# Kernel optimization log

Measured on AMD Instinct MI355X. Metric: run time of the kernel, lower is better.

Reference implementation:

```python
import jax, jax.numpy as jnp
import numpy as np

# N nodes, E edges; lmax=6 -> L=(lmax+1)^2=49; lmax_reduce=(lmax+1)//2=3 -> LR=16
# (matches hardcoded c[:, :16, :] in the torch source); M=25 is the basis size of the
# lmax=4 'middle' irreps in cg_interaction2; NY = num_y_rotations.
# node_interaction's reshape(b, basis_num, c) forces sphere_channels_reduce == hidden_channels.
N, E, L, LR, M, NY, C, H, NB = 2048, 4096, 49, 16, 25, 3, 128, 128, 128
INV_SQRT_3 = float(1.0 / np.sqrt(3.0))


def _silu(v):
    return v * jax.nn.sigmoid(v)


def setup_inputs():
    key = jax.random.key(0)
    ks = jax.random.split(key, 24)
    rn = lambda k, s, sc=1.0: (sc * jax.random.normal(k, s)).astype(jnp.float32)
    return {
        "x": rn(ks[0], (N, L, C)),
        "x_time": rn(ks[1], (1, 1)),        # forward sets x_time = None; unused
        "x_glovec": rn(ks[2], (N, LR)),
        "x_edge": rn(ks[3], (E, NB)),
        "edge_index": jax.random.randint(ks[4], (2, E), 0, N),
        "edge_vec": rn(ks[5], (E, 3)),      # unused by forward body
        "node_sh_inv": rn(ks[6], (1,)),     # unused by forward body
        "node_self": rn(ks[7], (1,)),       # unused by forward body
        # dense bilinear stand-ins for the e3nn FullyConnectedTensorProducts
        "W_cg1": rn(ks[8], (L, L, M), 0.05),
        "W_cg21": rn(ks[9], (L, M, L), 0.05),
        "W_cg22": rn(ks[10], (L, M, L), 0.05),
        # node_interaction1 MLP
        "Wn1a": rn(ks[11], (LR * (C + 1), H), (LR * (C + 1)) ** -0.5),
        "bn1a": jnp.zeros((H,), jnp.float32),
        "Wn1b": rn(ks[12], (H, LR * C), H ** -0.5),
        "bn1b": jnp.zeros((LR * C,), jnp.float32),
        # node_interaction2 MLP
        "Wn2a": rn(ks[13], (LR * (C + 1), H), (LR * (C + 1)) ** -0.5),
        "bn2a": jnp.zeros((H,), jnp.float32),
        "Wn2b": rn(ks[14], (H, LR * C), H ** -0.5),
        "bn2b": jnp.zeros((LR * C,), jnp.float32),
        # fc1_dist / fc1_edge_proj / fc2_edge
        "Wd": rn(ks[15], (NB, H), NB ** -0.5),
        "bd": jnp.zeros((H,), jnp.float32),
        "Wp1": rn(ks[16], (LR * C, H), (LR * C) ** -0.5),
        "bp1": jnp.zeros((H,), jnp.float32),
        "Wp2": rn(ks[17], (H, LR * C), H ** -0.5),
        "bp2": jnp.zeros((LR * C,), jnp.float32),
        # per-edge Wigner-style rotation buffers (geometry-derived in the original)
        "wigner": rn(ks[18], (E, NY, LR, L), L ** -0.5),      # Rotate: full -> reduced, NY taps
        "wigner_inv": rn(ks[19], (E, L, LR), LR ** -0.5),     # RotateInv: reduced -> full
        "wig_node": rn(ks[20], (E, LR, LR), LR ** -0.5),      # Rotate_edge / Rotate_edgeInv
    }


def _forward(x, x_glovec, x_edge, W_cg1, W_cg21, W_cg22, Wn1a, bn1a, Wn1b, bn1b,
             Wn2a, bn2a, Wn2b, bn2b, Wd, bd, Wp1, bp1, Wp2, bp2,
             wigner, wigner_inv, wig_node, edge_index):
    src, dst = edge_index[0], edge_index[1]
    xe = _silu(x_edge @ Wd + bd)                              # [E,H]  fc1_dist
    xs, xt = x[src], x[dst]                                   # [E,L,C] edge gathers
    gs, gt = x_glovec[src], x_glovec[dst]                     # [E,LR]

    # cg_interaction2: mean over channels, CG bilinears, broadcast residual
    xm, ym = xs.mean(2), xt.mean(2)                           # [E,L]
    mid = jnp.einsum('ei,ej,ijo->eo', xm, ym, W_cg1)          # [E,M]  cg1
    sh_cg = xs + xt \
        + jnp.einsum('ei,ej,ijo->eo', xm, mid, W_cg21)[..., None] \
        + jnp.einsum('ei,ej,ijo->eo', ym, mid, W_cg22)[..., None]  # [E,L,C]

    def node_int(ne, ndf, Wa, ba, Wb, bb):
        # Rotate_edgeInv (transpose of per-edge rotation) on reduced basis
        ne = jnp.einsum('eji,ejc->eic', wig_node, ne[:, :LR, :])       # [E,LR,C]
        feat = jnp.concatenate([ne, (ne.mean(2) * ndf)[..., None]], axis=2)
        h = _silu(feat.reshape(E, LR * (C + 1)) @ Wa + ba)             # node_fc1
        h = _silu(h @ Wb + bb).reshape(E, LR, C)                       # node_fc3
        return jnp.einsum('eij,ejc->eic', wig_node, h)                 # Rotate_edge

    sh = node_int(xs, gt, Wn1a, bn1a, Wn1b, bn1b) \
       + node_int(xt, gs, Wn2a, bn2a, Wn2b, bn2b)                      # [E,LR,C]
    c = sh_cg.at[:, :LR, :].add(sh)

    def rotate(z):  # sphharm.Rotate: [E,L,C] -> [E*NY, LR*C]
        return jnp.einsum('enrb,ebc->enrc', wigner, z).reshape(E * NY, LR * C)

    msg = rotate(xs) + rotate(xt) + rotate(c)
    m = _silu(msg @ Wp1 + bp1)                                # [E*NY,H] fc1_edge_proj
    m = (m.reshape(E, NY, H) * xe[:, None, :]).reshape(E * NY, H)
    m = _silu(m @ Wp2 + bp2)                                  # fc2_edge
    m = m.reshape(E, NY, LR, C).mean(1)                       # CombineYRotations
    out = jnp.einsum('ebr,erc->ebc', wigner_inv, m) * INV_SQRT_3  # RotateInv
    return out                                                # [E,L,C]


def reference(x, x_time, x_glovec, x_edge, edge_index, edge_vec, node_sh_inv,
              node_self, W_cg1, W_cg21, W_cg22, Wn1a, bn1a, Wn1b, bn1b,
              Wn2a, bn2a, Wn2b, bn2b, Wd, bd, Wp1, bp1, Wp2, bp2,
              wigner, wigner_inv, wig_node):
    # x_time / edge_vec / node_sh_inv / node_self are unused (x_time = None in source)
    return _forward(x, x_glovec, x_edge, W_cg1, W_cg21, W_cg22, Wn1a, bn1a, Wn1b,
                    bn1b, Wn2a, bn2a, Wn2b, bn2b, Wd, bd, Wp1, bp1, Wp2, bp2,
                    wigner, wigner_inv, wig_node, edge_index)
```

## Files before the change

### kernel.cpp

```cpp
#include <hip/hip_runtime.h>
#include <hip/hip_bf16.h>

typedef __hip_bfloat16 bf16;
typedef __attribute__((ext_vector_type(8))) short short8;
typedef __attribute__((ext_vector_type(4))) float f32x4;

#define NN 2048
#define EE 4096
#define LL 49
#define LRR 16
#define NYY 3
#define CC 128
#define HH 128

#define K1P 2432
#define K2P 2496

__device__ __forceinline__ float siluf(float v) { return v * (1.0f / (1.0f + __expf(-v))); }
__device__ __forceinline__ bf16 f2b(float v) { return __float2bfloat16(v); }
__device__ __forceinline__ float getc(float4 v, int i) {
  return i == 0 ? v.x : i == 1 ? v.y : i == 2 ? v.z : v.w;
}

struct TJob { const float* in; bf16* out; int K, N, Kp; };
struct TJobs { TJob j[6]; };

__global__ __launch_bounds__(256) void transpose_cvt_kernel(TJobs jobs) {
  TJob jb = jobs.j[blockIdx.y];
  int i = blockIdx.x * 256 + threadIdx.x;
  if (i < jb.N * jb.Kp) {
    int n = i / jb.Kp, k = i - n * jb.Kp;
    jb.out[i] = (k < jb.K) ? f2b(jb.in[(long)k * jb.N + n]) : f2b(0.f);
  }
}

__global__ __launch_bounds__(256) void cg_prep_kernel(
    const float* __restrict__ Wcg1, const float* __restrict__ Wcg21,
    const float* __restrict__ Wcg22, bf16* __restrict__ BT1, bf16* __restrict__ BT2) {
  int i = blockIdx.x * 256 + threadIdx.x;
  if (blockIdx.y == 0) {
    if (i < 32 * K1P) {
      int o = i / K1P, k = i - o * K1P;
      float v = (o < 25 && k < 2401) ? Wcg1[k * 25 + o] : 0.f;
      BT1[i] = f2b(v);
    }
  } else {
    if (i < 64 * K2P) {
      int o = i / K2P, k = i - o * K2P;
      float v = 0.f;
      if (o < 49) {
        if (k < 1225) v = Wcg21[k * 49 + o];
        else if (k < 2450) v = Wcg22[(k - 1225) * 49 + o];
      }
      BT2[i] = f2b(v);
    }
  }
}

__global__ __launch_bounds__(256) void node_mean_kernel(const float* __restrict__ x,
                                                        float* __restrict__ xmean) {
  int row = blockIdx.x * 4 + (threadIdx.x >> 6);
  int lane = threadIdx.x & 63;
  const float* p = x + (long)row * CC;
  float s = p[lane] + p[lane + 64];
  for (int off = 32; off > 0; off >>= 1) s += __shfl_down(s, off);
  if (lane == 0) xmean[row] = s * (1.0f / 128.0f);
}

__global__ __launch_bounds__(256) void build_p1_kernel(
    const float* __restrict__ xmean, const int* __restrict__ eidx, bf16* __restrict__ P1) {
  __shared__ float sxm[49], sym[49];
  int e = blockIdx.x, tid = threadIdx.x;
  int s = eidx[e], d = eidx[EE + e];
  if (tid < 49) { sxm[tid] = xmean[s * 49 + tid]; sym[tid] = xmean[d * 49 + tid]; }
  __syncthreads();
  for (int idx = tid; idx < K1P; idx += 256) {
    float v = 0.f;
    if (idx < 2401) { int i = idx / 49, j = idx - i * 49; v = sxm[i] * sym[j]; }
    P1[(long)e * K1P + idx] = f2b(v);
  }
}

__global__ __launch_bounds__(256) void build_p2_kernel(
    const float* __restrict__ xmean, const float* __restrict__ mid,
    const int* __restrict__ eidx, bf16* __restrict__ P2) {
  __shared__ float sxm[49], sym[49], smid[25];
  int e = blockIdx.x, tid = threadIdx.x;
  int s = eidx[e], d = eidx[EE + e];
  if (tid < 49) { sxm[tid] = xmean[s * 49 + tid]; sym[tid] = xmean[d * 49 + tid]; }
  if (tid >= 64 && tid < 89) smid[tid - 64] = mid[e * 32 + tid - 64];
  __syncthreads();
  for (int idx = tid; idx < K2P; idx += 256) {
    float v = 0.f;
    if (idx < 1225) { int i = idx / 25, m = idx - i * 25; v = sxm[i] * smid[m]; }
    else if (idx < 2450) { int kk = idx - 1225; int i = kk / 25, m = kk - i * 25; v = sym[i] * smid[m]; }
    P2[(long)e * K2P + idx] = f2b(v);
  }
}

template <int NI>
__global__ __launch_bounds__(256) void gemm_smalln(
    const bf16* __restrict__ A, const bf16* __restrict__ BT,
    float* __restrict__ C, int K) {
  __shared__ short As[64 * 64];
  __shared__ short Bs[NI * 16 * 64];
  const int tid = threadIdx.x, w = tid >> 6, lane = tid & 63;
  const int lm = lane & 15, q = lane >> 4;
  const int bm = blockIdx.x * 64;
  f32x4 acc[NI];
#pragma unroll
  for (int ni = 0; ni < NI; ++ni) acc[ni] = (f32x4){0.f, 0.f, 0.f, 0.f};
  for (int k0 = 0; k0 < K; k0 += 64) {
    __syncthreads();
#pragma unroll
    for (int it = 0; it < 2; ++it) {
      int lc = it * 256 + tid;
      int m = lc >> 3, k8 = lc & 7;
      uint4 v = *(const uint4*)((const char*)A + ((long)(bm + m) * K + k0 + k8 * 8) * 2);
      *(uint4*)&As[(m * 8 + (k8 ^ (m & 7))) * 8] = v;
    }
#pragma unroll
    for (int it = 0; it < NI / 2; ++it) {
      int lc = it * 256 + tid;
      int n = lc >> 3, k8 = lc & 7;
      uint4 v = *(const uint4*)((const char*)BT + ((long)n * K + k0 + k8 * 8) * 2);
      *(uint4*)&Bs[(n * 8 + (k8 ^ (n & 7))) * 8] = v;
    }
    __syncthreads();
#pragma unroll
    for (int ks = 0; ks < 2; ++ks) {
      short8 af = *(const short8*)&As[(w * 16 + lm) * 64 + ((ks * 4 + q) ^ (lm & 7)) * 8];
#pragma unroll
      for (int ni = 0; ni < NI; ++ni) {
        short8 bfr = *(const short8*)&Bs[(ni * 16 + lm) * 64 + ((ks * 4 + q) ^ (lm & 7)) * 8];
        acc[ni] = __builtin_amdgcn_mfma_f32_16x16x32_bf16(af, bfr, acc[ni], 0, 0, 0);
      }
    }
  }
#pragma unroll
  for (int ni = 0; ni < NI; ++ni) {
    int col = ni * 16 + lm;
#pragma unroll
    for (int r = 0; r < 4; ++r) {
      int row = bm + w * 16 + q * 4 + r;
      C[(long)row * (NI * 16) + col] = acc[ni][r];
    }
  }
}

__global__ __launch_bounds__(256) void build_feat_kernel(
    const float* __restrict__ x, const float* __restrict__ x_glovec,
    const float* __restrict__ wig_node, const int* __restrict__ eidx,
    bf16* __restrict__ featst) {
  __shared__ float wig[256];
  __shared__ float xa[2048], xb[2048], tmp[2048];
  int e = blockIdx.x, tid = threadIdx.x;
  int s = eidx[e], d = eidx[EE + e];
  wig[tid] = wig_node[e * 256 + tid];
  if (tid < 48) {
    featst[(long)e * 2112 + 2064 + tid] = f2b(0.f);
    featst[(long)(EE + e) * 2112 + 2064 + tid] = f2b(0.f);
  }
  for (int idx = tid; idx < 2048; idx += 256) {
    int l = idx >> 7, c = idx & 127;
    xa[idx] = x[((long)s * LL + l) * CC + c];
    xb[idx] = x[((long)d * LL + l) * CC + c];
  }
  __syncthreads();
  for (int idx = tid; idx < 2048; idx += 256) {
    int i = idx >> 7, c = idx & 127;
    float a = 0.f;
#pragma unroll
    for (int j = 0; j < 16; ++j) a += wig[j * 16 + i] * xa[j * 128 + c];
    tmp[idx] = a;
    featst[(long)e * 2112 + i * 129 + c] = f2b(a);
  }
  __syncthreads();
  if (tid < 16) {
    float m = 0.f;
    for (int c = 0; c < 128; ++c) m += tmp[tid * 128 + c];
    featst[(long)e * 2112 + tid * 129 + 128] = f2b(m * (1.0f / 128.0f) * x_glovec[(long)d * 16 + tid]);
  }
  __syncthreads();
  for (int idx = tid; idx < 2048; idx += 256) {
    int i = idx >> 7, c = idx & 127;
    float a = 0.f;
#pragma unroll
    for (int j = 0; j < 16; ++j) a += wig[j * 16 + i] * xb[j * 128 + c];
    tmp[idx] = a;
    featst[(long)(EE + e) * 2112 + i * 129 + c] = f2b(a);
  }
  __syncthreads();
  if (tid < 16) {
    float m = 0.f;
    for (int c = 0; c < 128; ++c) m += tmp[tid * 128 + c];
    featst[(long)(EE + e) * 2112 + tid * 129 + 128] = f2b(m * (1.0f / 128.0f) * x_glovec[(long)s * 16 + tid]);
  }
}

__global__ __launch_bounds__(256) void gemm_f32_silu(
    const float* __restrict__ A, const float* __restrict__ B,
    const float* __restrict__ bias, float* __restrict__ C, int M, int N, int K) {
  __shared__ float As[16][68];
  __shared__ float Bs[16][64];
  const int tid = threadIdx.x;
  const int bm = blockIdx.x * 64, bn = blockIdx.y * 64;
  const int tx = tid & 15, ty = tid >> 4;
  const int ar = tid >> 2, ak = (tid & 3) * 4;
  const int br = tid >> 4, bc = (tid & 15) * 4;
  float acc[4][4] = {};
  const float* Ap = A + (long)(bm + ar) * K + ak;
  const float* Bp = B + (long)br * N + bn + bc;
  for (int k0 = 0; k0 < K; k0 += 16) {
    const float4 av = *(const float4*)(Ap + k0);
    const float4 bv = *(const float4*)(Bp + (long)k0 * N);
    __syncthreads();
    As[ak + 0][ar] = av.x; As[ak + 1][ar] = av.y;
    As[ak + 2][ar] = av.z; As[ak + 3][ar] = av.w;
    *(float4*)&Bs[br][bc] = bv;
    __syncthreads();
#pragma unroll
    for (int k = 0; k < 16; ++k) {
      const float4 a = *(const float4*)&As[k][ty * 4];
      const float4 b = *(const float4*)&Bs[k][tx * 4];
      acc[0][0] += a.x * b.x; acc[0][1] += a.x * b.y; acc[0][2] += a.x * b.z; acc[0][3] += a.x * b.w;
      acc[1][0] += a.y * b.x; acc[1][1] += a.y * b.y; acc[1][2] += a.y * b.z; acc[1][3] += a.y * b.w;
      acc[2][0] += a.z * b.x; acc[2][1] += a.z * b.y; acc[2][2] += a.z * b.z; acc[2][3] += a.z * b.w;
      acc[3][0] += a.w * b.x; acc[3][1] += a.w * b.y; acc[3][2] += a.w * b.z; acc[3][3] += a.w * b.w;
    }
  }
#pragma unroll
  for (int i = 0; i < 4; ++i) {
    int row = bm + ty * 4 + i;
#pragma unroll
    for (int j = 0; j < 4; ++j) {
      int col = bn + tx * 4 + j;
      C[(long)row * N + col] = siluf(acc[i][j] + bias[col]);
    }
  }
}

template <int BM, bool SILU, bool XE, bool OUT_BF16>
__global__ __launch_bounds__(256) void gemm_mfma(
    const bf16* __restrict__ A, const bf16* __restrict__ B0, const bf16* __restrict__ B1,
    const float* __restrict__ bias0, const float* __restrict__ bias1,
    const float* __restrict__ xe, void* __restrict__ Cout,
    int M, int N, int K, int half) {
  constexpr int MI = BM / 32;
  __shared__ short As[BM * 64];
  __shared__ short Bs[128 * 64];
  const int tid = threadIdx.x;
  const int w = tid >> 6, lane = tid & 63;
  const int lm = lane & 15, q = lane >> 4;
  const int bm = blockIdx.x * BM, bn = blockIdx.y * 128;
  const int wm = (w & 1) * (BM / 2), wn = (w >> 1) * 64;
  const bf16* Bp = (bm < half) ? B0 : B1;
  const float* bias = (bm < half) ? bias0 : bias1;

  f32x4 acc[MI][4];
#pragma unroll
  for (int mi = 0; mi < MI; ++mi)
#pragma unroll
    for (int ni = 0; ni < 4; ++ni) acc[mi][ni] = (f32x4){0.f, 0.f, 0.f, 0.f};

  for (int k0 = 0; k0 < K; k0 += 64) {
    __syncthreads();
#pragma unroll
    for (int it = 0; it < BM / 32; ++it) {
      int lc = it * 256 + tid;
      int m = lc >> 3, k8 = lc & 7;
      uint4 v = *(const uint4*)((const char*)A + ((long)(bm + m) * K + k0 + k8 * 8) * 2);
      *(uint4*)&As[(m * 8 + (k8 ^ (m & 7))) * 8] = v;
    }
#pragma unroll
    for (int it = 0; it < 4; ++it) {
      int lc = it * 256 + tid;
      int n = lc >> 3, k8 = lc & 7;
      uint4 v = *(const uint4*)((const char*)Bp + ((long)(bn + n) * K + k0 + k8 * 8) * 2);
      *(uint4*)&Bs[(n * 8 + (k8 ^ (n & 7))) * 8] = v;
    }
    __syncthreads();
#pragma unroll
    for (int ks = 0; ks < 2; ++ks) {
      short8 af[MI], bfr[4];
#pragma unroll
      for (int mi = 0; mi < MI; ++mi) {
        int row = wm + mi * 16 + lm;
        af[mi] = *(const short8*)&As[row * 64 + ((ks * 4 + q) ^ (lm & 7)) * 8];
      }
#pragma unroll
      for (int ni = 0; ni < 4; ++ni) {
        int row = wn + ni * 16 + lm;
        bfr[ni] = *(const short8*)&Bs[row * 64 + ((ks * 4 + q) ^ (lm & 7)) * 8];
      }
#pragma unroll
      for (int mi = 0; mi < MI; ++mi)
#pragma unroll
        for (int ni = 0; ni < 4; ++ni)
          acc[mi][ni] = __builtin_amdgcn_mfma_f32_16x16x32_bf16(af[mi], bfr[ni], acc[mi][ni], 0, 0, 0);
    }
  }
#pragma unroll
  for (int mi = 0; mi < MI; ++mi) {
#pragma unroll
    for (int ni = 0; ni < 4; ++ni) {
      int col = bn + wn + ni * 16 + lm;
      float bcol = bias[col];
#pragma unroll
      for (int r = 0; r < 4; ++r) {
        int row = bm + wm + mi * 16 + q * 4 + r;
        float v = acc[mi][ni][r] + bcol;
        if (SILU) v = siluf(v);
        if (XE) v *= xe[(row / 3) * HH + col];
        if (OUT_BF16) ((bf16*)Cout)[(long)row * N + col] = f2b(v);
        else ((float*)Cout)[(long)row * N + col] = v;
      }
    }
  }
}

__global__ __launch_bounds__(256) void gemm_osum(
    const bf16* __restrict__ A, const bf16* __restrict__ B0w, const bf16* __restrict__ B1w,
    const float* __restrict__ bias0, const float* __restrict__ bias1,
    float* __restrict__ osum) {
  __shared__ short As[128 * 64];
  __shared__ short Bs[128 * 64];
  const int tid = threadIdx.x;
  const int w = tid >> 6, lane = tid & 63;
  const int lm = lane & 15, q = lane >> 4;
  const int bm = blockIdx.x * 128, bn = blockIdx.y * 128;
  const int wm = (w & 1) * 64, wn = (w >> 1) * 64;
  f32x4 ov[4][4];
  f32x4 acc[4][4];
#pragma unroll
  for (int mi = 0; mi < 4; ++mi)
#pragma unroll
    for (int ni = 0; ni < 4; ++ni) acc[mi][ni] = (f32x4){0.f, 0.f, 0.f, 0.f};

#pragma unroll 1
  for (int src = 0; src < 2; ++src) {
    const bf16* Ap = A + (long)src * 4096 * 128;
    const bf16* Bp = src ? B1w : B0w;
#pragma unroll 1
    for (int k0 = 0; k0 < 128; k0 += 64) {
      __syncthreads();
#pragma unroll
      for (int it = 0; it < 4; ++it) {
        int lc = it * 256 + tid;
        int m = lc >> 3, k8 = lc & 7;
        uint4 v = *(const uint4*)((const char*)Ap + ((long)(bm + m) * 128 + k0 + k8 * 8) * 2);
        *(uint4*)&As[(m * 8 + (k8 ^ (m & 7))) * 8] = v;
      }
#pragma unroll
      for (int it = 0; it < 4; ++it) {
        int lc = it * 256 + tid;
        int n = lc >> 3, k8 = lc & 7;
        uint4 v = *(const uint4*)((const char*)Bp + ((long)(bn + n) * 128 + k0 + k8 * 8) * 2);
        *(uint4*)&Bs[(n * 8 + (k8 ^ (n & 7))) * 8] = v;
      }
      __syncthreads();
#pragma unroll
      for (int ks = 0; ks < 2; ++ks) {
        short8 af[4], bfr[4];
#pragma unroll
        for (int mi = 0; mi < 4; ++mi)
          af[mi] = *(const short8*)&As[(wm + mi * 16 + lm) * 64 + ((ks * 4 + q) ^ (lm & 7)) * 8];
#pragma unroll
        for (int ni = 0; ni < 4; ++ni)
          bfr[ni] = *(const short8*)&Bs[(wn + ni * 16 + lm) * 64 + ((ks * 4 + q) ^ (lm & 7)) * 8];
#pragma unroll
        for (int mi = 0; mi < 4; ++mi)
#pragma unroll
          for (int ni = 0; ni < 4; ++ni)
            acc[mi][ni] = __builtin_amdgcn_mfma_f32_16x16x32_bf16(af[mi], bfr[ni], acc[mi][ni], 0, 0, 0);
      }
    }
    if (src == 0) {
#pragma unroll
      for (int mi = 0; mi < 4; ++mi)
#pragma unroll
        for (int ni = 0; ni < 4; ++ni) {
          int col = bn + wn + ni * 16 + lm;
          float bc = bias0[col];
#pragma unroll
          for (int r = 0; r < 4; ++r) ov[mi][ni][r] = siluf(acc[mi][ni][r] + bc);
#pragma unroll
          for (int r = 0; r < 4; ++r) acc[mi][ni][r] = 0.f;
        }
    }
  }
#pragma unroll
  for (int mi = 0; mi < 4; ++mi)
#pragma unroll
    for (int ni = 0; ni < 4; ++ni) {
      int col = bn + wn + ni * 16 + lm;
      float bc = bias1[col];
#pragma unroll
      for (int r = 0; r < 4; ++r) {
        int row = bm + wm + mi * 16 + q * 4 + r;
        osum[(long)row * 2048 + col] = ov[mi][ni][r] + siluf(acc[mi][ni][r] + bc);
      }
    }
}

__global__ __launch_bounds__(512, 4) void rotate_msg_fused_kernel(
    const float* __restrict__ x, const float* __restrict__ wigner,
    const int* __restrict__ eidx, const float* __restrict__ asum,
    const float* __restrict__ osum, const float* __restrict__ wig_node,
    bf16* __restrict__ msg) {
  __shared__ bf16 Ah[48 * 64], Al[48 * 64];
  __shared__ bf16 zTh[128 * 64], zTl[128 * 64];
  __shared__ float z[49 * 132];
  __shared__ float osum_s[16 * 128];
  __shared__ float wig[256];
  __shared__ float as_s[49];
  const int e = blockIdx.x, tid = threadIdx.x;
  const int s = eidx[e], d = eidx[EE + e];
  const int w = tid >> 6, lane = tid & 63;
  const int lm = lane & 15, q = lane >> 4;

  if (tid < 49) as_s[tid] = asum[e * 64 + tid];
  if (tid >= 64 && tid < 128) {
    int i = tid - 64;
    *(float4*)&wig[i * 4] = *(const float4*)&wig_node[(long)e * 256 + i * 4];
  }
  *(float4*)&osum_s[tid * 4] = *(const float4*)&osum[(long)e * 2048 + tid * 4];
  for (int i = tid; i < 48 * 15; i += 512) {
    int m = i / 15, k = 49 + (i - m * 15);
    int off = m * 64 + (((k >> 3) ^ (m & 7)) << 3) + (k & 7);
    Ah[off] = f2b(0.f); Al[off] = f2b(0.f);
  }
  for (int i4 = tid; i4 < 588; i4 += 512) {
    float4 v4 = *(const float4*)&wigner[(long)e * 2352 + i4 * 4];
    int i = i4 * 4;
    int m = i / 49, k = i - m * 49;
    float vv[4] = {v4.x, v4.y, v4.z, v4.w};
#pragma unroll
    for (int j = 0; j < 4; ++j) {
      bf16 h = f2b(vv[j]);
      bf16 l = f2b(vv[j] - __bfloat162float(h));
      int off = m * 64 + (((k >> 3) ^ (m & 7)) << 3) + (k & 7);
      Ah[off] = h; Al[off] = l;
      if (++k == 49) { k = 0; ++m; }
    }
  }
  __syncthreads();

  {
    const float* xs = x + (long)s * (LL * CC);
    const float* xt = x + (long)d * (LL * CC);
    for (int i4 = tid; i4 < 49 * 32; i4 += 512) {
      int l = i4 >> 5, c4 = i4 & 31;
      float4 a = *(const float4*)&xs[l * 128 + c4 * 4];
      float4 b = *(const float4*)&xt[l * 128 + c4 * 4];
      float ad = as_s[l];
      float4 v;
      v.x = 2.f * (a.x + b.x) + ad;
      v.y = 2.f * (a.y + b.y) + ad;
      v.z = 2.f * (a.z + b.z) + ad;
      v.w = 2.f * (a.w + b.w) + ad;
      if (l < 16) {
#pragma unroll
        for (int j = 0; j < 16; ++j) {
          float wv = wig[l * 16 + j];
          float4 o = *(const float4*)&osum_s[j * 128 + c4 * 4];
          v.x += wv * o.x; v.y += wv * o.y; v.z += wv * o.z; v.w += wv * o.w;
        }
      }
      *(float4*)&z[l * 132 + c4 * 4] = v;
    }
  }
  __syncthreads();

  {
    const int b0 = (tid & 15) * 4;
    const int c0 = (tid >> 4) * 4;
    float4 rv[4];
#pragma unroll
    for (int j = 0; j < 4; ++j)
      rv[j] = (b0 + j < 49) ? *(const float4*)&z[(b0 + j) * 132 + c0]
                            : (float4){0.f, 0.f, 0.f, 0.f};
#pragma unroll
    for (int i = 0; i < 4; ++i) {
      int c = c0 + i;
      union { bf16 b[4]; unsigned long long u; } hu, lu;
#pragma unroll
      for (int j = 0; j < 4; ++j) {
        float v = getc(rv[j], i);
        bf16 h = f2b(v);
        hu.b[j] = h;
        lu.b[j] = f2b(v - __bfloat162float(h));
      }
      int off = c * 64 + (((b0 >> 3) ^ (c & 7)) << 3) + (b0 & 7);
      *(unsigned long long*)&zTh[off] = hu.u;
      *(unsigned long long*)&zTl[off] = lu.u;
    }
  }
  __syncthreads();

  short8 ah[3][2], alo[3][2], bh[2], bl[2];
#pragma unroll
  for (int mi = 0; mi < 3; ++mi)
#pragma unroll
    for (int ks = 0; ks < 2; ++ks) {
      int off = (mi * 16 + lm) * 64 + (((ks * 4 + q) ^ (lm & 7)) << 3);
      ah[mi][ks] = *(const short8*)&Ah[off];
      alo[mi][ks] = *(const short8*)&Al[off];
    }
#pragma unroll
  for (int ks = 0; ks < 2; ++ks) {
    int off = (w * 16 + lm) * 64 + (((ks * 4 + q) ^ (lm & 7)) << 3);
    bh[ks] = *(const short8*)&zTh[off];
    bl[ks] = *(const short8*)&zTl[off];
  }
  f32x4 acc[3];
#pragma unroll
  for (int mi = 0; mi < 3; ++mi) acc[mi] = (f32x4){0.f, 0.f, 0.f, 0.f};
#pragma unroll
  for (int mi = 0; mi < 3; ++mi)
#pragma unroll
    for (int ks = 0; ks < 2; ++ks) {
      acc[mi] = __builtin_amdgcn_mfma_f32_16x16x32_bf16(ah[mi][ks], bh[ks], acc[mi], 0, 0, 0);
      acc[mi] = __builtin_amdgcn_mfma_f32_16x16x32_bf16(ah[mi][ks], bl[ks], acc[mi], 0, 0, 0);
      acc[mi] = __builtin_amdgcn_mfma_f32_16x16x32_bf16(alo[mi][ks], bh[ks], acc[mi], 0, 0, 0);
    }
  {
    int c = w * 16 + lm;
#pragma unroll
    for (int mi = 0; mi < 3; ++mi) {
      long base = ((long)e * 3 + mi) * 2048 + c;
#pragma unroll
      for (int r = 0; r < 4; ++r)
        msg[base + (q * 4 + r) * 128] = f2b(acc[mi][r]);
    }
  }
}

__global__ __launch_bounds__(512) void m2out_kernel(
    const bf16* __restrict__ m1, const bf16* __restrict__ BTp2,
    const float* __restrict__ bp2, const float* __restrict__ wigner_inv,
    float* __restrict__ out) {
  __shared__ __align__(16) char sm[4096 + 32768 + 8448 + 32768];
  short (*As)[1024] = (short(*)[1024])sm;
  short (*Bs)[8192] = (short(*)[8192])(sm + 4096);
  float* pbuf = (float*)(sm + 4096 + 32768);
  float* mr   = (float*)(sm + 4096 + 32768 + 8448);
  float* wv_s = (float*)(sm + 4096);

  const int tid = threadIdx.x;
  const int w = tid >> 6, lane = tid & 63;
  const int lm = lane & 15, q = lane >> 4;
  const int e0 = blockIdx.x * 4;

  if (tid < 256) {
    int n = tid >> 4, k8 = tid & 15;
    uint4 v = (uint4){0, 0, 0, 0};
    if (n < 12) v = *(const uint4*)((const char*)m1 + ((long)(e0 * 3 + n) * 128 + k8 * 8) * 2);
    *(uint4*)&As[k8 >> 3][(n * 8 + ((k8 & 7) ^ (n & 7))) * 8] = v;
  }

#pragma unroll 1
  for (int nc = 0; nc < 16; ++nc) {
    __syncthreads();
#pragma unroll
    for (int it = 0; it < 4; ++it) {
      int lc = it * 512 + tid;
      int n = lc >> 4, k8 = lc & 15;
      uint4 v = *(const uint4*)((const char*)BTp2 + ((long)(nc * 128 + n) * 128 + k8 * 8) * 2);
      *(uint4*)&Bs[k8 >> 3][(n * 8 + ((k8 & 7) ^ (n & 7))) * 8] = v;
    }
    __syncthreads();
    f32x4 acc = (f32x4){0.f, 0.f, 0.f, 0.f};
#pragma unroll
    for (int ks = 0; ks < 4; ++ks) {
      int kh = ks >> 1, ksl = ks & 1;
      short8 af = *(const short8*)&As[kh][(lm * 8 + ((ksl * 4 + q) ^ (lm & 7))) * 8];
      int brow = w * 16 + lm;
      short8 bfr = *(const short8*)&Bs[kh][(brow * 8 + ((ksl * 4 + q) ^ (brow & 7))) * 8];
      acc = __builtin_amdgcn_mfma_f32_16x16x32_bf16(af, bfr, acc, 0, 0, 0);
    }
    {
      int col = w * 16 + lm;
      float bc = bp2[nc * 128 + col];
#pragma unroll
      for (int r = 0; r < 4; ++r)
        pbuf[(q * 4 + r) * 132 + col] = siluf(acc[r] + bc);
    }
    __syncthreads();
    {
      int c = tid & 127, e4 = tid >> 7;
      mr[e4 * 2048 + nc * 128 + c] =
          (pbuf[(3 * e4 + 0) * 132 + c] + pbuf[(3 * e4 + 1) * 132 + c] +
           pbuf[(3 * e4 + 2) * 132 + c]) * (1.f / 3.f);
    }
  }
  __syncthreads();
  for (int i4 = tid; i4 < 784; i4 += 512)
    *(float4*)&wv_s[i4 * 4] = *(const float4*)&wigner_inv[(long)e0 * 784 + i4 * 4];
  __syncthreads();
  {
    const int c4 = tid & 31, sb = (tid >> 5) & 3, ep = tid >> 7;
#pragma unroll 1
    for (int bb = 0; bb < 13; ++bb) {
      int b = bb * 4 + sb;
      if (b < 49) {
        float a0 = 0.f, a1 = 0.f, a2 = 0.f, a3 = 0.f;
#pragma unroll
        for (int r = 0; r < 16; ++r) {
          float wvv = wv_s[ep * 784 + b * 16 + r];
          const float4 m = *(const float4*)&mr[ep * 2048 + r * 128 + c4 * 4];
          a0 += wvv * m.x; a1 += wvv * m.y; a2 += wvv * m.z; a3 += wvv * m.w;
        }
        float4 o;
        o.x = a0 * 0.57735026918962576f; o.y = a1 * 0.57735026918962576f;
        o.z = a2 * 0.57735026918962576f; o.w = a3 * 0.57735026918962576f;
        *(float4*)&out[(long)(e0 + ep) * 6272 + b * 128 + c4 * 4] = o;
      }
    }
  }
}

extern "C" void kernel_launch(void* const* d_in, const int* in_sizes, int n_in,
                              void* d_out, int out_size, void* d_ws, size_t ws_size,
                              hipStream_t stream) {
  (void)in_sizes; (void)n_in; (void)out_size; (void)ws_size;
  const float* x        = (const float*)d_in[0];
  const float* x_glovec = (const float*)d_in[2];
  const float* x_edge   = (const float*)d_in[3];
  const int*   eidx     = (const int*)d_in[4];
  const float* W_cg1   = (const float*)d_in[8];
  const float* W_cg21  = (const float*)d_in[9];
  const float* W_cg22  = (const float*)d_in[10];
  const float* Wn1a = (const float*)d_in[11];
  const float* bn1a = (const float*)d_in[12];
  const float* Wn1b = (const float*)d_in[13];
  const float* bn1b = (const float*)d_in[14];
  const float* Wn2a = (const float*)d_in[15];
  const float* bn2a = (const float*)d_in[16];
  const float* Wn2b = (const float*)d_in[17];
  const float* bn2b = (const float*)d_in[18];
  const float* Wd   = (const float*)d_in[19];
  const float* bd   = (const float*)d_in[20];
  const float* Wp1  = (const float*)d_in[21];
  const float* bp1  = (const float*)d_in[22];
  const float* Wp2  = (const float*)d_in[23];
  const float* bp2  = (const float*)d_in[24];
  const float* wigner     = (const float*)d_in[25];
  const float* wigner_inv = (const float*)d_in[26];
  const float* wig_node   = (const float*)d_in[27];

  char* W = (char*)d_ws;
  bf16*  featst = (bf16*)(W + 0);
  float* p_osum = (float*)(W + 34603008);
  bf16*  msg    = (bf16*)(W + 135266304);
  bf16*  P1     = (bf16*)(W + 135266304);
  bf16*  P2     = (bf16*)(W + 155189248);
  bf16*  hstack = (bf16*)(W + 185597952);
  bf16*  m1     = (bf16*)(W + 187695104);
  float* p_xe   = (float*)(W + 190840832);
  float* p_xmean= (float*)(W + 192937984);
  bf16*  BTa    = (bf16*)(W + 194142208);
  bf16*  BTb    = (bf16*)(W + 195223552);
  bf16*  BTp1   = (bf16*)(W + 196272128);
  bf16*  BTp2   = (bf16*)(W + 196796416);
  float* p_asum = (float*)(W + 197320704);
  float* p_mid  = (float*)(W + 198369280);
  bf16*  BT1    = (bf16*)(W + 198893568);
  bf16*  BT2    = (bf16*)(W + 199049216);

  TJobs tj;
  tj.j[0] = {Wn1a, BTa,            2064, 128, 2112};
  tj.j[1] = {Wn2a, BTa + 270336,   2064, 128, 2112};
  tj.j[2] = {Wn1b, BTb,            128, 2048, 128};
  tj.j[3] = {Wn2b, BTb + 262144,   128, 2048, 128};
  tj.j[4] = {Wp1,  BTp1,           2048, 128, 2048};
  tj.j[5] = {Wp2,  BTp2,           128, 2048, 128};
  transpose_cvt_kernel<<<dim3(1056, 6), 256, 0, stream>>>(tj);
  cg_prep_kernel<<<dim3(624, 2), 256, 0, stream>>>(W_cg1, W_cg21, W_cg22, BT1, BT2);

  node_mean_kernel<<<(NN * LL) / 4, 256, 0, stream>>>(x, p_xmean);
  build_p1_kernel<<<EE, 256, 0, stream>>>(p_xmean, eidx, P1);
  gemm_smalln<2><<<EE / 64, 256, 0, stream>>>(P1, BT1, p_mid, K1P);
  build_p2_kernel<<<EE, 256, 0, stream>>>(p_xmean, p_mid, eidx, P2);
  gemm_smalln<4><<<EE / 64, 256, 0, stream>>>(P2, BT2, p_asum, K2P);

  gemm_f32_silu<<<dim3(EE / 64, 2), 256, 0, stream>>>(x_edge, Wd, bd, p_xe, EE, HH, 128);
  build_feat_kernel<<<EE, 256, 0, stream>>>(x, x_glovec, wig_node, eidx, featst);
  gemm_mfma<64, true, false, true><<<dim3(128, 1), 256, 0, stream>>>(
      featst, BTa, BTa + 270336, bn1a, bn2a, nullptr, hstack, 8192, 128, 2112, 4096);
  gemm_osum<<<dim3(32, 16), 256, 0, stream>>>(hstack, BTb, BTb + 262144, bn1b, bn2b, p_osum);
  rotate_msg_fused_kernel<<<EE, 512, 0, stream>>>(
      x, wigner, eidx, p_asum, p_osum, wig_node, msg);
  gemm_mfma<64, true, true, true><<<dim3(192, 1), 256, 0, stream>>>(
      msg, BTp1, BTp1, bp1, bp1, p_xe, m1, 12288, 128, 2048, 1 << 30);
  m2out_kernel<<<EE / 4, 512, 0, stream>>>(m1, BTp2, bp2, wigner_inv, (float*)d_out);
}
```

Measured before the change: 569.6 us.

## Fuse CG outer-product builds into GEMMs and restructure m2out, smaller GEMM tiles

The separate P1/P2 build kernels and small-N GEMMs are replaced by cg1/cg2 kernels that form the outer-product A tiles directly in shared memory, so the large bf16 P1/P2 intermediates are never written to or read from global memory. m2out now prefetches the next B chunk into registers and folds the inverse-Wigner rotation into a per-thread 49-element register accumulator instead of staging it through shared memory. build_feat gets vectorised loads and a parallel shuffle reduction for the row means. The two main mfma GEMMs switch to 32-row tiles with twice as many blocks, trading per-block reuse for more parallelism, and m2out now carries higher register pressure.

New measurement: 656.5 us. 1.15x slower.

```diff
diff --git a/kernel.cpp b/kernel.cpp
--- a/kernel.cpp
+++ b/kernel.cpp
@@ -67,85 +67,122 @@
   if (lane == 0) xmean[row] = s * (1.0f / 128.0f);
 }
 
-__global__ __launch_bounds__(256) void build_p1_kernel(
-    const float* __restrict__ xmean, const int* __restrict__ eidx, bf16* __restrict__ P1) {
-  __shared__ float sxm[49], sym[49];
-  int e = blockIdx.x, tid = threadIdx.x;
-  int s = eidx[e], d = eidx[EE + e];
-  if (tid < 49) { sxm[tid] = xmean[s * 49 + tid]; sym[tid] = xmean[d * 49 + tid]; }
-  __syncthreads();
-  for (int idx = tid; idx < K1P; idx += 256) {
-    float v = 0.f;
-    if (idx < 2401) { int i = idx / 49, j = idx - i * 49; v = sxm[i] * sym[j]; }
-    P1[(long)e * K1P + idx] = f2b(v);
-  }
-}
-
-__global__ __launch_bounds__(256) void build_p2_kernel(
-    const float* __restrict__ xmean, const float* __restrict__ mid,
-    const int* __restrict__ eidx, bf16* __restrict__ P2) {
-  __shared__ float sxm[49], sym[49], smid[25];
-  int e = blockIdx.x, tid = threadIdx.x;
-  int s = eidx[e], d = eidx[EE + e];
-  if (tid < 49) { sxm[tid] = xmean[s * 49 + tid]; sym[tid] = xmean[d * 49 + tid]; }
-  if (tid >= 64 && tid < 89) smid[tid - 64] = mid[e * 32 + tid - 64];
-  __syncthreads();
-  for (int idx = tid; idx < K2P; idx += 256) {
-    float v = 0.f;
-    if (idx < 1225) { int i = idx / 25, m = idx - i * 25; v = sxm[i] * smid[m]; }
-    else if (idx < 2450) { int kk = idx - 1225; int i = kk / 25, m = kk - i * 25; v = sym[i] * smid[m]; }
-    P2[(long)e * K2P + idx] = f2b(v);
-  }
-}
-
-template <int NI>
-__global__ __launch_bounds__(256) void gemm_smalln(
-    const bf16* __restrict__ A, const bf16* __restrict__ BT,
-    float* __restrict__ C, int K) {
-  __shared__ short As[64 * 64];
-  __shared__ short Bs[NI * 16 * 64];
+__global__ __launch_bounds__(256) void cg1_kernel(
+    const float* __restrict__ xmean, const int* __restrict__ eidx,
+    const bf16* __restrict__ BT1, float* __restrict__ mid) {
+  __shared__ float sxm[32 * 49], sym[32 * 49];
+  __shared__ bf16 As[32 * 64];
+  __shared__ bf16 Bs[32 * 64];
+  __shared__ int se[32], de[32];
   const int tid = threadIdx.x, w = tid >> 6, lane = tid & 63;
   const int lm = lane & 15, q = lane >> 4;
-  const int bm = blockIdx.x * 64;
-  f32x4 acc[NI];
-#pragma unroll
-  for (int ni = 0; ni < NI; ++ni) acc[ni] = (f32x4){0.f, 0.f, 0.f, 0.f};
-  for (int k0 = 0; k0 < K; k0 += 64) {
-    __syncthreads();
+  const int e0 = blockIdx.x * 32;
+  if (tid < 32) { se[tid] = eidx[e0 + tid]; de[tid] = eidx[EE + e0 + tid]; }
+  __syncthreads();
+  for (int i = tid; i < 32 * 49; i += 256) {
+    int m = i / 49, l = i - m * 49;
+    sxm[i] = xmean[se[m] * 49 + l];
+    sym[i] = xmean[de[m] * 49 + l];
+  }
+  const int mi = w >> 1, ni = w & 1;
+  f32x4 acc = (f32x4){0.f, 0.f, 0.f, 0.f};
+  for (int k0 = 0; k0 < K1P; k0 += 64) {
+    __syncthreads();
+    for (int idx = tid; idx < 2048; idx += 256) {
+      int m = idx >> 6, kk = idx & 63;
+      int k = k0 + kk;
+      float v = 0.f;
+      if (k < 2401) { int i = k / 49, j = k - i * 49; v = sxm[m * 49 + i] * sym[m * 49 + j]; }
+      int k8 = kk >> 3;
+      As[(m * 8 + (k8 ^ (m & 7))) * 8 + (kk & 7)] = f2b(v);
+    }
+    {
+      int n = tid >> 3, k8 = tid & 7;
+      uint4 v = *(const uint4*)((const char*)BT1 + ((long)n * K1P + k0 + k8 * 8) * 2);
+      *(uint4*)&Bs[(n * 8 + (k8 ^ (n & 7))) * 8] = v;
+    }
+    __syncthreads();
+#pragma unroll
+    for (int ks = 0; ks < 2; ++ks) {
+      int am = mi * 16 + lm, bn = ni * 16 + lm;
+      short8 af = *(const short8*)&As[(am * 8 + ((ks * 4 + q) ^ (am & 7))) * 8];
+      short8 bfr = *(const short8*)&Bs[(bn * 8 + ((ks * 4 + q) ^ (bn & 7))) * 8];
+      acc = __builtin_amdgcn_mfma_f32_16x16x32_bf16(af, bfr, acc, 0, 0, 0);
+    }
+  }
+#pragma unroll
+  for (int r = 0; r < 4; ++r)
+    mid[(long)(e0 + mi * 16 + q * 4 + r) * 32 + ni * 16 + lm] = acc[r];
+}
+
+__global__ __launch_bounds__(256) void cg2_kernel(
+    const float* __restrict__ xmean, const float* __restrict__ mid,
+    const int* __restrict__ eidx, const bf16* __restrict__ BT2,
+    float* __restrict__ asum) {
+  __shared__ float sxm[32 * 49], sym[32 * 49], smid[32 * 25];
+  __shared__ bf16 As[32 * 64];
+  __shared__ bf16 Bs[64 * 64];
+  __shared__ int se[32], de[32];
+  const int tid = threadIdx.x, w = tid >> 6, lane = tid & 63;
+  const int lm = lane & 15, q = lane >> 4;
+  const int e0 = blockIdx.x * 32;
+  if (tid < 32) { se[tid] = eidx[e0 + tid]; de[tid] = eidx[EE + e0 + tid]; }
+  __syncthreads();
+  for (int i = tid; i < 32 * 49; i += 256) {
+    int m = i / 49, l = i - m * 49;
+    sxm[i] = xmean[se[m] * 49 + l];
+    sym[i] = xmean[de[m] * 49 + l];
+  }
+  for (int i = tid; i < 32 * 25; i += 256) {
+    int m = i / 25, l = i - m * 25;
+    smid[i] = mid[(long)(e0 + m) * 32 + l];
+  }
+  const int ni = w;
+  f32x4 acc[2];
+  acc[0] = (f32x4){0.f, 0.f, 0.f, 0.f};
+  acc[1] = (f32x4){0.f, 0.f, 0.f, 0.f};
+  for (int k0 = 0; k0 < K2P; k0 += 64) {
+    __syncthreads();
+    for (int idx = tid; idx < 2048; idx += 256) {
+      int m = idx >> 6, kk = idx & 63;
+      int k = k0 + kk;
+      float v = 0.f;
+      if (k < 1225) {
+        int i = k / 25, mm = k - i * 25;
+        v = sxm[m * 49 + i] * smid[m * 25 + mm];
+      } else if (k < 2450) {
+        int kk2 = k - 1225;
+        int i = kk2 / 25, mm = kk2 - i * 25;
+        v = sym[m * 49 + i] * smid[m * 25 + mm];
+      }
+      int k8 = kk >> 3;
+      As[(m * 8 + (k8 ^ (m & 7))) * 8 + (kk & 7)] = f2b(v);
+    }
 #pragma unroll
     for (int it = 0; it < 2; ++it) {
       int lc = it * 256 + tid;
-      int m = lc >> 3, k8 = lc & 7;
-      uint4 v = *(const uint4*)((const char*)A + ((long)(bm + m) * K + k0 + k8 * 8) * 2);
-      *(uint4*)&As[(m * 8 + (k8 ^ (m & 7))) * 8] = v;
-    }
-#pragma unroll
-    for (int it = 0; it < NI / 2; ++it) {
-      int lc = it * 256 + tid;
       int n = lc >> 3, k8 = lc & 7;
-      uint4 v = *(const uint4*)((const char*)BT + ((long)n * K + k0 + k8 * 8) * 2);
+      uint4 v = *(const uint4*)((const char*)BT2 + ((long)n * K2P + k0 + k8 * 8) * 2);
       *(uint4*)&Bs[(n * 8 + (k8 ^ (n & 7))) * 8] = v;
     }
     __syncthreads();
 #pragma unroll
     for (int ks = 0; ks < 2; ++ks) {
-      short8 af = *(const short8*)&As[(w * 16 + lm) * 64 + ((ks * 4 + q) ^ (lm & 7)) * 8];
-#pragma unroll
-      for (int ni = 0; ni < NI; ++ni) {
-        short8 bfr = *(const short8*)&Bs[(ni * 16 + lm) * 64 + ((ks * 4 + q) ^ (lm & 7)) * 8];
-        acc[ni] = __builtin_amdgcn_mfma_f32_16x16x32_bf16(af, bfr, acc[ni], 0, 0, 0);
-      }
-    }
-  }
-#pragma unroll
-  for (int ni = 0; ni < NI; ++ni) {
-    int col = ni * 16 + lm;
-#pragma unroll
-    for (int r = 0; r < 4; ++r) {
-      int row = bm + w * 16 + q * 4 + r;
-      C[(long)row * (NI * 16) + col] = acc[ni][r];
-    }
-  }
+      int bn = ni * 16 + lm;
+      short8 bfr = *(const short8*)&Bs[(bn * 8 + ((ks * 4 + q) ^ (bn & 7))) * 8];
+#pragma unroll
+      for (int mi = 0; mi < 2; ++mi) {
+        int am = mi * 16 + lm;
+        short8 af = *(const short8*)&As[(am * 8 + ((ks * 4 + q) ^ (am & 7))) * 8];
+        acc[mi] = __builtin_amdgcn_mfma_f32_16x16x32_bf16(af, bfr, acc[mi], 0, 0, 0);
+      }
+    }
+  }
+#pragma unroll
+  for (int mi = 0; mi < 2; ++mi)
+#pragma unroll
+    for (int r = 0; r < 4; ++r)
+      asum[(long)(e0 + mi * 16 + q * 4 + r) * 64 + ni * 16 + lm] = acc[mi][r];
 }
 
 __global__ __launch_bounds__(256) void build_feat_kernel(
@@ -161,10 +198,10 @@
     featst[(long)e * 2112 + 2064 + tid] = f2b(0.f);
     featst[(long)(EE + e) * 2112 + 2064 + tid] = f2b(0.f);
   }
-  for (int idx = tid; idx < 2048; idx += 256) {
-    int l = idx >> 7, c = idx & 127;
-    xa[idx] = x[((long)s * LL + l) * CC + c];
-    xb[idx] = x[((long)d * LL + l) * CC + c];
+  for (int i4 = tid; i4 < 512; i4 += 256) {
+    int l = i4 >> 5, c4 = i4 & 31;
+    *(float4*)&xa[l * 128 + c4 * 4] = *(const float4*)&x[((long)s * LL + l) * CC + c4 * 4];
+    *(float4*)&xb[l * 128 + c4 * 4] = *(const float4*)&x[((long)d * LL + l) * CC + c4 * 4];
   }
   __syncthreads();
   for (int idx = tid; idx < 2048; idx += 256) {
@@ -176,10 +213,18 @@
     featst[(long)e * 2112 + i * 129 + c] = f2b(a);
   }
   __syncthreads();
-  if (tid < 16) {
+  {
+    int row = tid >> 4, t = tid & 15;
     float m = 0.f;
-    for (int c = 0; c < 128; ++c) m += tmp[tid * 128 + c];
-    featst[(long)e * 2112 + tid * 129 + 128] = f2b(m * (1.0f / 128.0f) * x_glovec[(long)d * 16 + tid]);
+#pragma unroll
+    for (int k = 0; k < 8; ++k) m += tmp[row * 128 + t + k * 16];
+    m += __shfl_down(m, 8, 16);
+    m += __shfl_down(m, 4, 16);
+    m += __shfl_down(m, 2, 16);
+    m += __shfl_down(m, 1, 16);
+    if (t == 0)
+      featst[(long)e * 2112 + row * 129 + 128] =
+          f2b(m * (1.0f / 128.0f) * x_glovec[(long)d * 16 + row]);
   }
   __syncthreads();
   for (int idx = tid; idx < 2048; idx += 256) {
@@ -191,10 +236,18 @@
     featst[(long)(EE + e) * 2112 + i * 129 + c] = f2b(a);
   }
   __syncthreads();
-  if (tid < 16) {
+  {
+    int row = tid >> 4, t = tid & 15;
     float m = 0.f;
-    for (int c = 0; c < 128; ++c) m += tmp[tid * 128 + c];
-    featst[(long)(EE + e) * 2112 + tid * 129 + 128] = f2b(m * (1.0f / 128.0f) * x_glovec[(long)s * 16 + tid]);
+#pragma unroll
+    for (int k = 0; k < 8; ++k) m += tmp[row * 128 + t + k * 16];
+    m += __shfl_down(m, 8, 16);
+    m += __shfl_down(m, 4, 16);
+    m += __shfl_down(m, 2, 16);
+    m += __shfl_down(m, 1, 16);
+    if (t == 0)
+      featst[(long)(EE + e) * 2112 + row * 129 + 128] =
+          f2b(m * (1.0f / 128.0f) * x_glovec[(long)s * 16 + row]);
   }
 }
 
@@ -246,7 +299,7 @@
     const float* __restrict__ bias0, const float* __restrict__ bias1,
     const float* __restrict__ xe, void* __restrict__ Cout,
     int M, int N, int K, int half) {
-  constexpr int MI = BM / 32;
+  constexpr int MI = (BM + 31) / 32;
   __shared__ short As[BM * 64];
   __shared__ short Bs[128 * 64];
   const int tid = threadIdx.x;
@@ -540,17 +593,15 @@
     const bf16* __restrict__ m1, const bf16* __restrict__ BTp2,
     const float* __restrict__ bp2, const float* __restrict__ wigner_inv,
     float* __restrict__ out) {
-  __shared__ __align__(16) char sm[4096 + 32768 + 8448 + 32768];
-  short (*As)[1024] = (short(*)[1024])sm;
-  short (*Bs)[8192] = (short(*)[8192])(sm + 4096);
-  float* pbuf = (float*)(sm + 4096 + 32768);
-  float* mr   = (float*)(sm + 4096 + 32768 + 8448);
-  float* wv_s = (float*)(sm + 4096);
-
+  __shared__ short As[2][16 * 64];
+  __shared__ short Bs[2][128 * 64];
+  __shared__ float pbuf[16 * 132];
+  __shared__ float wvp[4][16 * 52];
   const int tid = threadIdx.x;
   const int w = tid >> 6, lane = tid & 63;
   const int lm = lane & 15, q = lane >> 4;
   const int e0 = blockIdx.x * 4;
+  const int ep = tid >> 7, cc = tid & 127;
 
   if (tid < 256) {
     int n = tid >> 4, k8 = tid & 15;
@@ -558,16 +609,39 @@
     if (n < 12) v = *(const uint4*)((const char*)m1 + ((long)(e0 * 3 + n) * 128 + k8 * 8) * 2);
     *(uint4*)&As[k8 >> 3][(n * 8 + ((k8 & 7) ^ (n & 7))) * 8] = v;
   }
+  for (int i = tid; i < 3136; i += 512) {
+    int ep2 = i / 784, r = i - ep2 * 784;
+    int b = r >> 4, rr = r & 15;
+    wvp[ep2][rr * 52 + b] = wigner_inv[(long)e0 * 784 + i];
+  }
+
+  float oacc[49];
+#pragma unroll
+  for (int b = 0; b < 49; ++b) oacc[b] = 0.f;
+
+  uint4 bv[4];
+#pragma unroll
+  for (int it = 0; it < 4; ++it) {
+    int lc = it * 512 + tid;
+    int n = lc >> 4, k8 = lc & 15;
+    bv[it] = *(const uint4*)((const char*)BTp2 + ((long)n * 128 + k8 * 8) * 2);
+  }
 
 #pragma unroll 1
   for (int nc = 0; nc < 16; ++nc) {
-    __syncthreads();
 #pragma unroll
     for (int it = 0; it < 4; ++it) {
       int lc = it * 512 + tid;
       int n = lc >> 4, k8 = lc & 15;
-      uint4 v = *(const uint4*)((const char*)BTp2 + ((long)(nc * 128 + n) * 128 + k8 * 8) * 2);
-      *(uint4*)&Bs[k8 >> 3][(n * 8 + ((k8 & 7) ^ (n & 7))) * 8] = v;
+      *(uint4*)&Bs[k8 >> 3][(n * 8 + ((k8 & 7) ^ (n & 7))) * 8] = bv[it];
+    }
+    if (nc < 15) {
+#pragma unroll
+      for (int it = 0; it < 4; ++it) {
+        int lc = it * 512 + tid;
+        int n = lc >> 4, k8 = lc & 15;
+        bv[it] = *(const uint4*)((const char*)BTp2 + ((long)((nc + 1) * 128 + n) * 128 + k8 * 8) * 2);
+      }
     }
     __syncthreads();
     f32x4 acc = (f32x4){0.f, 0.f, 0.f, 0.f};
@@ -588,36 +662,24 @@
     }
     __syncthreads();
     {
-      int c = tid & 127, e4 = tid >> 7;
-      mr[e4 * 2048 + nc * 128 + c] =
-          (pbuf[(3 * e4 + 0) * 132 + c] + pbuf[(3 * e4 + 1) * 132 + c] +
-           pbuf[(3 * e4 + 2) * 132 + c]) * (1.f / 3.f);
-    }
-  }
-  __syncthreads();
-  for (int i4 = tid; i4 < 784; i4 += 512)
-    *(float4*)&wv_s[i4 * 4] = *(const float4*)&wigner_inv[(long)e0 * 784 + i4 * 4];
-  __syncthreads();
-  {
-    const int c4 = tid & 31, sb = (tid >> 5) & 3, ep = tid >> 7;
-#pragma unroll 1
-    for (int bb = 0; bb < 13; ++bb) {
-      int b = bb * 4 + sb;
-      if (b < 49) {
-        float a0 = 0.f, a1 = 0.f, a2 = 0.f, a3 = 0.f;
-#pragma unroll
-        for (int r = 0; r < 16; ++r) {
-          float wvv = wv_s[ep * 784 + b * 16 + r];
-          const float4 m = *(const float4*)&mr[ep * 2048 + r * 128 + c4 * 4];
-          a0 += wvv * m.x; a1 += wvv * m.y; a2 += wvv * m.z; a3 += wvv * m.w;
-        }
-        float4 o;
-        o.x = a0 * 0.57735026918962576f; o.y = a1 * 0.57735026918962576f;
-        o.z = a2 * 0.57735026918962576f; o.w = a3 * 0.57735026918962576f;
-        *(float4*)&out[(long)(e0 + ep) * 6272 + b * 128 + c4 * 4] = o;
-      }
-    }
-  }
+      float mv = (pbuf[(3 * ep + 0) * 132 + cc] + pbuf[(3 * ep + 1) * 132 + cc] +
+                  pbuf[(3 * ep + 2) * 132 + cc]) * (1.f / 3.f);
+      const float* wr = &wvp[ep][nc * 52];
+#pragma unroll
+      for (int b4 = 0; b4 < 12; ++b4) {
+        float4 w4 = *(const float4*)&wr[b4 * 4];
+        oacc[b4 * 4 + 0] += w4.x * mv;
+        oacc[b4 * 4 + 1] += w4.y * mv;
+        oacc[b4 * 4 + 2] += w4.z * mv;
+        oacc[b4 * 4 + 3] += w4.w * mv;
+      }
+      oacc[48] += wr[48] * mv;
+    }
+  }
+  const float s3 = 0.57735026918962576f;
+#pragma unroll
+  for (int b = 0; b < 49; ++b)
+    out[(long)(e0 + ep) * 6272 + b * 128 + cc] = oacc[b] * s3;
 }
 
 extern "C" void kernel_launch(void* const* d_in, const int* in_sizes, int n_in,
@@ -653,8 +715,6 @@
   bf16*  featst = (bf16*)(W + 0);
   float* p_osum = (float*)(W + 34603008);
   bf16*  msg    = (bf16*)(W + 135266304);
-  bf16*  P1     = (bf16*)(W + 135266304);
-  bf16*  P2     = (bf16*)(W + 155189248);
   bf16*  hstack = (bf16*)(W + 185597952);
   bf16*  m1     = (bf16*)(W + 187695104);
   float* p_xe   = (float*)(W + 190840832);
@@ -679,19 +739,17 @@
   cg_prep_kernel<<<dim3(624, 2), 256, 0, stream>>>(W_cg1, W_cg21, W_cg22, BT1, BT2);
 
   node_mean_kernel<<<(NN * LL) / 4, 256, 0, stream>>>(x, p_xmean);
-  build_p1_kernel<<<EE, 256, 0, stream>>>(p_xmean, eidx, P1);
-  gemm_smalln<2><<<EE / 64, 256, 0, stream>>>(P1, BT1, p_mid, K1P);
-  build_p2_kernel<<<EE, 256, 0, stream>>>(p_xmean, p_mid, eidx, P2);
-  gemm_smalln<4><<<EE / 64, 256, 0, stream>>>(P2, BT2, p_asum, K2P);
+  cg1_kernel<<<EE / 32, 256, 0, stream>>>(p_xmean, eidx, BT1, p_mid);
+  cg2_kernel<<<EE / 32, 256, 0, stream>>>(p_xmean, p_mid, eidx, BT2, p_asum);
 
   gemm_f32_silu<<<dim3(EE / 64, 2), 256, 0, stream>>>(x_edge, Wd, bd, p_xe, EE, HH, 128);
   build_feat_kernel<<<EE, 256, 0, stream>>>(x, x_glovec, wig_node, eidx, featst);
-  gemm_mfma<64, true, false, true><<<dim3(128, 1), 256, 0, stream>>>(
+  gemm_mfma<32, true, false, true><<<dim3(256, 1), 256, 0, stream>>>(
       featst, BTa, BTa + 270336, bn1a, bn2a, nullptr, hstack, 8192, 128, 2112, 4096);
   gemm_osum<<<dim3(32, 16), 256, 0, stream>>>(hstack, BTb, BTb + 262144, bn1b, bn2b, p_osum);
   rotate_msg_fused_kernel<<<EE, 512, 0, stream>>>(
       x, wigner, eidx, p_asum, p_osum, wig_node, msg);
-  gemm_mfma<64, true, true, true><<<dim3(192, 1), 256, 0, stream>>>(
+  gemm_mfma<32, true, true, true><<<dim3(384, 1), 256, 0, stream>>>(
       msg, BTp1, BTp1, bp1, bp1, p_xe, m1, 12288, 128, 2048, 1 << 30);
   m2out_kernel<<<EE / 4, 512, 0, stream>>>(m1, BTp2, bp2, wigner_inv, (float*)d_out);
 }
```
